# Kernel optimization log

Hardware: AMD Instinct MI355X
Metric: run time of the kernel (lower is better)

Reference implementation:

```python
import jax, jax.numpy as jnp
import numpy as np

B, N, C, H = 4, 2048, 384, 6
D = C // H                       # head_dim = 64
HID = 4 * C                      # mlp hidden = 1536
SCALE = D ** -0.5
EPS = 1e-5                       # torch nn.LayerNorm default


def setup_inputs() -> dict:
    key = jax.random.key(0)
    ks = jax.random.split(key, 8)
    s = 0.02
    return {
        "x": jax.random.normal(ks[0], (B, N, C), jnp.float32),
        "ln1_g": jnp.ones((C,), jnp.float32),
        "ln1_b": jnp.zeros((C,), jnp.float32),
        "w_qkv": jax.random.normal(ks[1], (3 * C, C), jnp.float32) * s,
        "w_proj": jax.random.normal(ks[2], (C, C), jnp.float32) * s,
        "b_proj": jnp.zeros((C,), jnp.float32),
        "ln2_g": jnp.ones((C,), jnp.float32),
        "ln2_b": jnp.zeros((C,), jnp.float32),
        "w_fc1": jax.random.normal(ks[3], (HID, C), jnp.float32) * s,
        "b_fc1": jnp.zeros((HID,), jnp.float32),
        "w_fc2": jax.random.normal(ks[4], (C, HID), jnp.float32) * s,
        "b_fc2": jnp.zeros((C,), jnp.float32),
    }


def _layernorm(x, g, b):
    mu = jnp.mean(x, axis=-1, keepdims=True)
    var = jnp.mean(jnp.square(x - mu), axis=-1, keepdims=True)
    return (x - mu) * jax.lax.rsqrt(var + EPS) * g + b


def _bf16_round(x):
    # emulate the .bfloat16() cast after each residual (precision truncation)
    return x.astype(jnp.bfloat16).astype(jnp.float32)


def reference(x, ln1_g, ln1_b, w_qkv, w_proj, b_proj,
              ln2_g, ln2_b, w_fc1, b_fc1, w_fc2, b_fc2):
    # ---- attention branch (quant=False => HMQ ops are pass-through) ----
    h = _layernorm(x, ln1_g, ln1_b)                       # [B,N,C]
    qkv = jnp.einsum('bnc,oc->bno', h, w_qkv)             # [B,N,3C]
    qkv = qkv.reshape(B, N, 3, H, D).transpose(2, 0, 3, 1, 4)  # [3,B,H,N,D]
    q, k, v = qkv[0], qkv[1], qkv[2]
    attn = jnp.einsum('bhnd,bhmd->bhnm', q, k) * SCALE    # [B,H,N,N]
    attn = jax.nn.softmax(attn, axis=-1)
    o = jnp.einsum('bhnm,bhmd->bhnd', attn, v)            # [B,H,N,D]
    o = o.transpose(0, 2, 1, 3).reshape(B, N, C)
    o = jnp.einsum('bnc,oc->bno', o, w_proj) + b_proj
    x = _bf16_round(x + o)

    # ---- MLP branch ----
    h = _layernorm(x, ln2_g, ln2_b)
    h = jnp.einsum('bnc,hc->bnh', h, w_fc1) + b_fc1       # [B,N,HID]
    h = jax.nn.gelu(h, approximate=False)
    h = jnp.einsum('bnh,ch->bnc', h, w_fc2) + b_fc2       # [B,N,C]
    x = _bf16_round(x + h)
    return x
```

## Files before the change

### kernel.cpp

```cpp
#include <hip/hip_runtime.h>
#include <cstdint>
#include <cstddef>

#define DI __device__ __forceinline__

typedef __attribute__((ext_vector_type(8))) short short8;
typedef __attribute__((ext_vector_type(4))) float f32x4;
typedef __attribute__((ext_vector_type(16))) float f32x16;
typedef unsigned int u32;
typedef unsigned short u16;

DI u16 rne_bf16(float f) {
  union { float f; u32 u; } v; v.f = f;
  u32 b = v.u;
  return (u16)((b + 0x7fffu + ((b >> 16) & 1u)) >> 16);
}
DI float bf2f(u16 h) {
  union { u32 u; float f; } v; v.u = ((u32)h) << 16;
  return v.f;
}
DI u32 cvtpk_bf16(float a, float b) {
  u32 r;
  asm("v_cvt_pk_bf16_f32 %0, %1, %2" : "=v"(r) : "v"(a), "v"(b));
  return r;
}

DI void gl2lds16(const void* g, void* l) {
  __builtin_amdgcn_global_load_lds(
      (const __attribute__((address_space(1))) u32*)g,
      (__attribute__((address_space(3))) u32*)l, 16, 0, 0);
}

DI void bar() {
  asm volatile("" ::: "memory");
  __builtin_amdgcn_s_barrier();
  asm volatile("" ::: "memory");
}

template<int ROWS, int NT>
DI void stage_swz(const u16* src, int ld, char* ldsb, int tid) {
  int wbase = tid & ~63;
  #pragma unroll
  for (int c = 0; c < (ROWS * 8) / NT; ++c) {
    int g = c * NT + tid;
    int row = g >> 3;
    int sgr = (g & 7) ^ (row & 7);
    gl2lds16(src + row * ld + sgr * 8, ldsb + (size_t)(c * NT + wbase) * 16);
  }
}

DI short8 lds_frag(const char* base, int row, int k0) {
  return *(const short8*)(base + row * 128 + ((k0 * 2) ^ ((row & 7) << 4)));
}

DI f32x4 mfma16(short8 a, short8 b, f32x4 c) {
  return __builtin_amdgcn_mfma_f32_16x16x32_bf16(a, b, c, 0, 0, 0);
}
DI f32x16 mfma32(short8 a, short8 b, f32x16 c) {
  return __builtin_amdgcn_mfma_f32_32x32x16_bf16(a, b, c, 0, 0, 0);
}

__global__ __launch_bounds__(256) void cvt_w(
    const float* __restrict__ a, const float* __restrict__ b,
    const float* __restrict__ c, const float* __restrict__ d,
    u16* __restrict__ oa, u16* __restrict__ ob, u16* __restrict__ oc,
    u16* __restrict__ od) {
  int i = blockIdx.x * 256 + threadIdx.x;
  if (i < 442368) oa[i] = rne_bf16(a[i]);
  else if (i < 589824) ob[i - 442368] = rne_bf16(b[i - 442368]);
  else if (i < 1179648) oc[i - 589824] = rne_bf16(c[i - 589824]);
  else if (i < 1769472) od[i - 1179648] = rne_bf16(d[i - 1179648]);
}

template<int INBF>
__global__ __launch_bounds__(256) void ln_k(
    const void* __restrict__ xin, const float* __restrict__ gam,
    const float* __restrict__ bet, u16* __restrict__ out) {
  int row = blockIdx.x * 4 + (threadIdx.x >> 6);
  int lane = threadIdx.x & 63;
  float v[6];
  if (INBF) {
    const u16* x = (const u16*)xin + (size_t)row * 384 + lane;
    #pragma unroll
    for (int j = 0; j < 6; ++j) v[j] = bf2f(x[j * 64]);
  } else {
    const float* x = (const float*)xin + (size_t)row * 384 + lane;
    #pragma unroll
    for (int j = 0; j < 6; ++j) v[j] = x[j * 64];
  }
  float s = 0.f;
  #pragma unroll
  for (int j = 0; j < 6; ++j) s += v[j];
  #pragma unroll
  for (int d = 1; d < 64; d <<= 1) s += __shfl_xor(s, d);
  float mu = s * (1.f / 384.f);
  float q = 0.f;
  #pragma unroll
  for (int j = 0; j < 6; ++j) { float t = v[j] - mu; q += t * t; }
  #pragma unroll
  for (int d = 1; d < 64; d <<= 1) q += __shfl_xor(q, d);
  float rstd = rsqrtf(q * (1.f / 384.f) + 1e-5f);
  #pragma unroll
  for (int j = 0; j < 6; ++j) {
    int c = j * 64 + lane;
    out[(size_t)row * 384 + c] = rne_bf16((v[j] - mu) * rstd * gam[c] + bet[c]);
  }
}

struct EpiP {
  const float* bias;
  const float* residf;
  const u16* residb;
  u16* outb;
  float* outf;
  u16* q; u16* k; u16* v;
};

#define QSCALE 0.18033688011112042f

template<int EPI, int MT>
__global__ __launch_bounds__(256) void gemm_bt(
    const u16* __restrict__ A, const u16* __restrict__ W, int K, int bnN,
    EpiP p) {
  constexpr int ABUF = MT * 128;
  constexpr int NC = (MT == 128) ? 4 : 2;
  __shared__ char lds[2 * (ABUF + 16384)];
  int tid = threadIdx.x, lane = tid & 63, wid = tid >> 6;
  int wr = (MT == 128) ? (wid >> 1) * 64 : 0;
  int wcb = (MT == 128) ? (wid & 1) * 64 : wid * 32;
  int fr = lane & 15, k8 = lane >> 4;
  int orig = blockIdx.x;
  int cpx = (int)gridDim.x >> 3;
  int wg = (orig & 7) * cpx + (orig >> 3);
  int bm = wg / bnN, bn = wg - bm * bnN;
  const u16* Ab = A + (size_t)bm * MT * K;
  const u16* Wb = W + (size_t)bn * 128 * K;

  stage_swz<MT, 256>(Ab, K, lds, tid);
  stage_swz<128, 256>(Wb, K, lds + ABUF, tid);

  f32x4 zz = {0.f, 0.f, 0.f, 0.f};
  f32x4 acc[4][NC];
  #pragma unroll
  for (int mr = 0; mr < 4; ++mr)
    #pragma unroll
    for (int nc = 0; nc < NC; ++nc) acc[mr][nc] = zz;

  asm volatile("s_waitcnt vmcnt(0)" ::: "memory");
  __syncthreads();

  int KT = K >> 6;
  for (int t = 0; t < KT; ++t) {
    char* base = lds + (size_t)(t & 1) * (ABUF + 16384);
    if (t + 1 < KT) {
      char* nb = lds + (size_t)((t + 1) & 1) * (ABUF + 16384);
      stage_swz<MT, 256>(Ab + (t + 1) * 64, K, nb, tid);
      stage_swz<128, 256>(Wb + (t + 1) * 64, K, nb + ABUF, tid);
    }
    #pragma unroll
    for (int ks = 0; ks < 2; ++ks) {
      int k0 = ks * 32 + k8 * 8;
      short8 av[4], bv[NC];
      #pragma unroll
      for (int mr = 0; mr < 4; ++mr) av[mr] = lds_frag(base, wr + mr * 16 + fr, k0);
      #pragma unroll
      for (int nc = 0; nc < NC; ++nc) bv[nc] = lds_frag(base + ABUF, wcb + nc * 16 + fr, k0);
      __builtin_amdgcn_s_setprio(1);
      #pragma unroll
      for (int mr = 0; mr < 4; ++mr)
        #pragma unroll
        for (int nc = 0; nc < NC; ++nc)
          acc[mr][nc] = mfma16(av[mr], bv[nc], acc[mr][nc]);
      __builtin_amdgcn_s_setprio(0);
    }
    if (t + 1 < KT) {
      asm volatile("s_waitcnt vmcnt(0)" ::: "memory");
      __syncthreads();
    }
  }

  #pragma unroll
  for (int mr = 0; mr < 4; ++mr)
    #pragma unroll
    for (int nc = 0; nc < NC; ++nc)
      #pragma unroll
      for (int r = 0; r < 4; ++r) {
        int m = bm * MT + wr + mr * 16 + k8 * 4 + r;
        int o = bn * 128 + wcb + nc * 16 + fr;
        float val = acc[mr][nc][r];
        if constexpr (EPI == 0) {
          int tq = o / 384;
          int rem = o - tq * 384;
          int hh = rem >> 6, d = rem & 63;
          int b = m >> 11, n = m & 2047;
          float sv = (tq == 0) ? val * QSCALE : val;
          u16 bvs = rne_bf16(sv);
          size_t qk = (((size_t)(b * 6 + hh)) * 2048 + n) * 64 + d;
          if (tq == 0) p.q[qk] = bvs;
          else if (tq == 1) p.k[qk] = bvs;
          else p.v[qk] = bvs;
        } else if constexpr (EPI == 1) {
          size_t idx = (size_t)m * 384 + o;
          float r2 = p.residf[idx] + val + p.bias[o];
          p.outb[idx] = rne_bf16(r2);
        } else if constexpr (EPI == 2) {
          size_t idx = (size_t)m * 1536 + o;
          float z = val + p.bias[o];
          float gl = 0.5f * z * (1.f + erff(z * 0.70710678118654752f));
          p.outb[idx] = rne_bf16(gl);
        } else {
          size_t idx = (size_t)m * 384 + o;
          float r2 = bf2f(p.residb[idx]) + val + p.bias[o];
          p.outf[idx] = bf2f(rne_bf16(r2));
        }
      }
}

__global__ __launch_bounds__(256) void vtr_k(
    const u16* __restrict__ v, u16* __restrict__ vt) {
  __shared__ u16 t[64 * 74];
  int tid = threadIdx.x;
  int n0 = blockIdx.x * 64, bh = blockIdx.y;
  const u16* src = v + ((size_t)bh * 2048 + n0) * 64;
  #pragma unroll
  for (int it = 0; it < 2; ++it) {
    int row = it * 32 + (tid >> 3), c8 = tid & 7;
    *(short8*)&t[row * 74 + c8 * 8] = *(const short8*)(src + row * 64 + c8 * 8);
  }
  __syncthreads();
  int dp = tid >> 3;
  int ng = tid & 7;
  u16 lo[8], hi[8];
  #pragma unroll
  for (int j = 0; j < 8; ++j) {
    u32 a = *(const u32*)&t[(ng * 8 + j) * 74 + dp * 2];
    lo[j] = (u16)a; hi[j] = (u16)(a >> 16);
  }
  u16* dst = vt + ((size_t)bh * 64 + 2 * dp) * 2048 + n0 + ng * 8;
  *(short8*)dst = *(short8*)&lo[0];
  *(short8*)(dst + 2048) = *(short8*)&hi[0];
}

__global__ __launch_bounds__(256) void attn_k(
    const u16* __restrict__ Qg, const u16* __restrict__ Kg,
    const u16* __restrict__ Vg, float* __restrict__ Op, float* __restrict__ lp) {
  __shared__ char lds[32768];
  int tid = threadIdx.x, lane = tid & 63, wid = tid >> 6;
  int l31 = lane & 31, h = lane >> 5;
  int qt = blockIdx.x, bh = blockIdx.y, z = blockIdx.z;
  const u16* Qb = Qg + (size_t)bh * 2048 * 64;
  const u16* Kb = Kg + ((size_t)bh * 2048 + z * 1024) * 64;
  const u16* Vb = Vg + (size_t)bh * 64 * 2048 + z * 1024;
  int qr0 = qt * 128 + wid * 32;

  short8 qf[4];
  #pragma unroll
  for (int m = 0; m < 4; ++m)
    qf[m] = *(const short8*)(Qb + (size_t)(qr0 + l31) * 64 + m * 16 + h * 8);

  f32x16 oacc[2];
  #pragma unroll
  for (int dt = 0; dt < 2; ++dt)
    #pragma unroll
    for (int r = 0; r < 16; ++r) oacc[dt][r] = 0.f;
  float lrun = 0.f;

  #define STAGE(t)                                                              \
    stage_swz<64, 256>(Kb + (size_t)(t) * 4096, 64, lds + ((t) & 1) * 8192, tid); \
    stage_swz<64, 256>(Vb + (t) * 64, 2048, lds + 16384 + ((t) & 1) * 8192, tid);

  STAGE(0);
  asm volatile("s_waitcnt vmcnt(0)" ::: "memory");
  bar();

  for (int t = 0; t < 16; ++t) {
    if (t + 1 < 16) { STAGE(t + 1); }
    char* kbase = lds + (t & 1) * 8192;
    char* vbase = lds + 16384 + (t & 1) * 8192;

    f32x16 s[2];
    #pragma unroll
    for (int kt = 0; kt < 2; ++kt) {
      #pragma unroll
      for (int r = 0; r < 16; ++r) s[kt][r] = 0.f;
      short8 kf[4];
      #pragma unroll
      for (int m = 0; m < 4; ++m)
        kf[m] = lds_frag(kbase, kt * 32 + l31, m * 16 + h * 8);
      __builtin_amdgcn_s_setprio(1);
      #pragma unroll
      for (int m = 0; m < 4; ++m) s[kt] = mfma32(kf[m], qf[m], s[kt]);
      __builtin_amdgcn_s_setprio(0);
    }
    #pragma unroll
    for (int kt = 0; kt < 2; ++kt)
      #pragma unroll
      for (int r = 0; r < 16; ++r) {
        float pv = exp2f(s[kt][r]);
        s[kt][r] = pv;
        lrun += pv;
      }
    #pragma unroll
    for (int kt = 0; kt < 2; ++kt) {
      u32 ow[4][2], pw[4][2];
      #pragma unroll
      for (int B = 0; B < 4; ++B) {
        ow[B][0] = cvtpk_bf16(s[kt][4 * B + 0], s[kt][4 * B + 1]);
        ow[B][1] = cvtpk_bf16(s[kt][4 * B + 2], s[kt][4 * B + 3]);
      }
      #pragma unroll
      for (int B = 0; B < 4; ++B) {
        pw[B][0] = __shfl_xor(ow[B][0], 32);
        pw[B][1] = __shfl_xor(ow[B][1], 32);
      }
      #pragma unroll
      for (int m = 0; m < 2; ++m) {
        union { u32 w[4]; short8 v; } af;
        af.w[0] = h ? pw[2 * m + 1][0] : ow[2 * m][0];
        af.w[1] = h ? pw[2 * m + 1][1] : ow[2 * m][1];
        af.w[2] = h ? ow[2 * m + 1][0] : pw[2 * m][0];
        af.w[3] = h ? ow[2 * m + 1][1] : pw[2 * m][1];
        int K0 = kt * 32 + m * 16;
        short8 vf0 = lds_frag(vbase, l31, K0 + h * 8);
        short8 vf1 = lds_frag(vbase, 32 + l31, K0 + h * 8);
        __builtin_amdgcn_s_setprio(1);
        oacc[0] = mfma32(af.v, vf0, oacc[0]);
        oacc[1] = mfma32(af.v, vf1, oacc[1]);
        __builtin_amdgcn_s_setprio(0);
      }
    }
    asm volatile("s_waitcnt vmcnt(0)" ::: "memory");
    if (t < 15) bar();
  }
  #undef STAGE

  float ltot = lrun + __shfl_xor(lrun, 32);
  size_t rowb = (size_t)z * 49152 + (size_t)bh * 2048;
  #pragma unroll
  for (int dt = 0; dt < 2; ++dt)
    #pragma unroll
    for (int r = 0; r < 16; ++r) {
      int qrow = qr0 + (r & 3) + 8 * (r >> 2) + 4 * h;
      Op[(rowb + qrow) * 64 + dt * 32 + l31] = oacc[dt][r];
    }
  if (lane < 32) lp[rowb + qr0 + l31] = ltot;
}

__global__ __launch_bounds__(256) void attn_merge(
    const float* __restrict__ Op, const float* __restrict__ lp,
    u16* __restrict__ ao) {
  int row = blockIdx.x * 4 + (threadIdx.x >> 6);
  int d = threadIdx.x & 63;
  float l = lp[row] + lp[49152 + row];
  float v = (Op[(size_t)row * 64 + d] + Op[(size_t)(49152 + row) * 64 + d]) / l;
  int bh = row >> 11, n = row & 2047;
  int b = bh / 6, hh = bh - b * 6;
  ao[((size_t)(b * 2048 + n)) * 384 + hh * 64 + d] = rne_bf16(v);
}

extern "C" void kernel_launch(void* const* d_in, const int* in_sizes, int n_in,
                              void* d_out, int out_size, void* d_ws, size_t ws_size,
                              hipStream_t stream) {
  const float* x     = (const float*)d_in[0];
  const float* ln1g  = (const float*)d_in[1];
  const float* ln1b  = (const float*)d_in[2];
  const float* wqkv  = (const float*)d_in[3];
  const float* wproj = (const float*)d_in[4];
  const float* bproj = (const float*)d_in[5];
  const float* ln2g  = (const float*)d_in[6];
  const float* ln2b  = (const float*)d_in[7];
  const float* wfc1  = (const float*)d_in[8];
  const float* bfc1  = (const float*)d_in[9];
  const float* wfc2  = (const float*)d_in[10];
  const float* bfc2  = (const float*)d_in[11];
  float* out = (float*)d_out;

  char* w = (char*)d_ws;
  u16* h1     = (u16*)w; w += 6291456;
  u16* x2     = (u16*)w; w += 6291456;
  u16* h2     = (u16*)w; w += 6291456;
  u16* qb     = (u16*)w; w += 6291456;
  u16* kb     = (u16*)w; w += 6291456;
  u16* vtb    = (u16*)w; w += 6291456;
  u16* ao     = (u16*)w; w += 6291456;
  u16* act    = (u16*)w; w += 25165824;
  u16* wqkvb  = (u16*)w; w += 884736;
  u16* wprojb = (u16*)w; w += 294912;
  u16* wfc1b  = (u16*)w; w += 1179648;
  u16* wfc2b  = (u16*)w; w += 1179648;

  u16* v_nat   = h2;
  float* Opart = (float*)act;
  float* lpart = (float*)h2;

  cvt_w<<<6912, 256, 0, stream>>>(wqkv, wproj, wfc1, wfc2, wqkvb, wprojb, wfc1b, wfc2b);
  ln_k<0><<<2048, 256, 0, stream>>>(x, ln1g, ln1b, h1);
  {
    EpiP p{}; p.q = qb; p.k = kb; p.v = v_nat;
    gemm_bt<0, 64><<<1152, 256, 0, stream>>>(h1, wqkvb, 384, 9, p);
  }
  vtr_k<<<dim3(32, 24), 256, 0, stream>>>(v_nat, vtb);
  attn_k<<<dim3(16, 24, 2), 256, 0, stream>>>(qb, kb, vtb, Opart, lpart);
  attn_merge<<<12288, 256, 0, stream>>>(Opart, lpart, ao);
  {
    EpiP p{}; p.bias = bproj; p.residf = x; p.outb = x2;
    gemm_bt<1, 64><<<384, 256, 0, stream>>>(ao, wprojb, 384, 3, p);
  }
  ln_k<1><<<2048, 256, 0, stream>>>(x2, ln2g, ln2b, h2);
  {
    EpiP p{}; p.bias = bfc1; p.outb = act;
    gemm_bt<2, 128><<<768, 256, 0, stream>>>(h2, wfc1b, 384, 12, p);
  }
  {
    EpiP p{}; p.bias = bfc2; p.residb = x2; p.outf = out;
    gemm_bt<3, 64><<<384, 256, 0, stream>>>(act, wfc2b, 1536, 3, p);
  }
}
```

Measured before the change: 228.9 us.

## Prefetch two tiles ahead with partial vmcnt waits in GEMM and attention

Restructures the double-buffered K-loops of the GEMM and flash-attention kernels to issue loads two tiles ahead. Each iteration now waits only for the older tile's loads using partial vmcnt counts, rather than draining all outstanding loads before the barrier. The aim is to keep more global memory traffic in flight so load latency overlaps the MFMA work. The cost is an extra barrier per iteration before restaging into the freed buffer. Correctness depends on the hardcoded vmcnt values matching the number of loads stage_swz issues per tile.

```diff
diff --git a/kernel.cpp b/kernel.cpp
--- a/kernel.cpp
+++ b/kernel.cpp
@@ -136,8 +136,14 @@
   const u16* Ab = A + (size_t)bm * MT * K;
   const u16* Wb = W + (size_t)bn * 128 * K;
 
-  stage_swz<MT, 256>(Ab, K, lds, tid);
-  stage_swz<128, 256>(Wb, K, lds + ABUF, tid);
+  #define GSTAGE(t)                                                            \
+    stage_swz<MT, 256>(Ab + (t) * 64, K,                                       \
+                       lds + (size_t)((t) & 1) * (ABUF + 16384), tid);         \
+    stage_swz<128, 256>(Wb + (t) * 64, K,                                      \
+                        lds + (size_t)((t) & 1) * (ABUF + 16384) + ABUF, tid);
+
+  GSTAGE(0);
+  GSTAGE(1);
 
   f32x4 zz = {0.f, 0.f, 0.f, 0.f};
   f32x4 acc[4][NC];
@@ -146,17 +152,16 @@
     #pragma unroll
     for (int nc = 0; nc < NC; ++nc) acc[mr][nc] = zz;
 
-  asm volatile("s_waitcnt vmcnt(0)" ::: "memory");
-  __syncthreads();
-
   int KT = K >> 6;
   for (int t = 0; t < KT; ++t) {
+    if (t + 1 < KT) {
+      if constexpr (MT == 128) asm volatile("s_waitcnt vmcnt(8)" ::: "memory");
+      else                     asm volatile("s_waitcnt vmcnt(6)" ::: "memory");
+    } else {
+      asm volatile("s_waitcnt vmcnt(0)" ::: "memory");
+    }
+    bar();
     char* base = lds + (size_t)(t & 1) * (ABUF + 16384);
-    if (t + 1 < KT) {
-      char* nb = lds + (size_t)((t + 1) & 1) * (ABUF + 16384);
-      stage_swz<MT, 256>(Ab + (t + 1) * 64, K, nb, tid);
-      stage_swz<128, 256>(Wb + (t + 1) * 64, K, nb + ABUF, tid);
-    }
     #pragma unroll
     for (int ks = 0; ks < 2; ++ks) {
       int k0 = ks * 32 + k8 * 8;
@@ -173,11 +178,12 @@
           acc[mr][nc] = mfma16(av[mr], bv[nc], acc[mr][nc]);
       __builtin_amdgcn_s_setprio(0);
     }
-    if (t + 1 < KT) {
-      asm volatile("s_waitcnt vmcnt(0)" ::: "memory");
-      __syncthreads();
-    }
-  }
+    if (t + 2 < KT) {
+      bar();
+      GSTAGE(t + 2);
+    }
+  }
+  #undef GSTAGE
 
   #pragma unroll
   for (int mr = 0; mr < 4; ++mr)
@@ -270,11 +276,12 @@
     stage_swz<64, 256>(Vb + (t) * 64, 2048, lds + 16384 + ((t) & 1) * 8192, tid);
 
   STAGE(0);
-  asm volatile("s_waitcnt vmcnt(0)" ::: "memory");
-  bar();
+  STAGE(1);
 
   for (int t = 0; t < 16; ++t) {
-    if (t + 1 < 16) { STAGE(t + 1); }
+    if (t + 1 < 16) { asm volatile("s_waitcnt vmcnt(4)" ::: "memory"); }
+    else            { asm volatile("s_waitcnt vmcnt(0)" ::: "memory"); }
+    bar();
     char* kbase = lds + (t & 1) * 8192;
     char* vbase = lds + 16384 + (t & 1) * 8192;
 
@@ -329,8 +336,10 @@
         __builtin_amdgcn_s_setprio(0);
       }
     }
-    asm volatile("s_waitcnt vmcnt(0)" ::: "memory");
-    if (t < 15) bar();
+    if (t + 2 < 16) {
+      bar();
+      STAGE(t + 2);
+    }
   }
   #undef STAGE
 
```

After: 228.3 us. Within noise of the previous version (-0.3%).
